# Optimization experiments

Measured on AMD Instinct MI355X. Metric: run time of the kernel, lower is better.

The kernel has to match this reference:

```python
import jax, jax.numpy as jnp
import numpy as np


def setup_inputs() -> dict:
    key = jax.random.key(0)
    k1, k2 = jax.random.split(key)
    # [1, D, H, W, C] cubic feature volume
    image_features = jax.random.normal(k1, (1, 64, 64, 64, 64), dtype=jnp.float32)
    # [1, N, 3] vertex coords in the original 128^3 volume, in [0, 128)
    graph_features = jax.random.uniform(k2, (1, 200000, 3), dtype=jnp.float32) * 128.0
    return {"image_features": image_features, "graph_features": graph_features}


def reference(image_features, graph_features):
    img = image_features[0]                      # [D, H, W, C]
    H = img.shape[0]
    factor = jnp.float32(128.0 / H)
    x = graph_features[..., -3] / factor         # [B, N]
    y = graph_features[..., -2] / factor
    z = graph_features[..., -1] / factor
    hm1 = jnp.float32(H - 1)
    x1 = jnp.floor(x); x2 = jnp.minimum(jnp.ceil(x), hm1)
    y1 = jnp.floor(y); y2 = jnp.minimum(jnp.ceil(y), hm1)
    z1 = jnp.floor(z); z2 = jnp.minimum(jnp.ceil(z), hm1)

    def gather(ix, iy, iz):
        # [B, N] index arrays -> [B, N, C] gathered features
        return img[ix.astype(jnp.int32), iy.astype(jnp.int32), iz.astype(jnp.int32)]

    wx = (x - x1)[..., None]; wx2 = (x2 - x)[..., None]
    wy = (y - y1)[..., None]; wy2 = (y2 - y)[..., None]
    wz = (z - z1)[..., None]; wz2 = (z2 - z)[..., None]

    # z = z1 plane
    q11 = gather(x1, y1, z1); q21 = gather(x2, y1, z1)
    q12 = gather(x1, y2, z1); q22 = gather(x2, y2, z1)
    lerp_y1 = (q22 * wx + q12 * wx2) * wy + (q21 * wx + q11 * wx2) * wy2

    # z = z2 plane
    q11 = gather(x1, y1, z2); q21 = gather(x2, y1, z2)
    q12 = gather(x1, y2, z2); q22 = gather(x2, y2, z2)
    lerp_y2 = (q22 * wx + q12 * wx2) * wy + (q21 * wx + q11 * wx2) * wy2

    return lerp_y2 * wz + lerp_y1 * wz2          # [B, N, C]
```

## Files before the change

kernel.cpp:

```cpp
#include <hip/hip_runtime.h>


#define NBUCK   4096
#define CAP     128
#define OVCAP   8192

typedef float __attribute__((ext_vector_type(4))) fx4;

__device__ __forceinline__ float4 f4mul(float4 a, float s) {
    return make_float4(a.x * s, a.y * s, a.z * s, a.w * s);
}
__device__ __forceinline__ float4 f4fma(float4 a, float s, float4 acc) {
    return make_float4(fmaf(a.x, s, acc.x), fmaf(a.y, s, acc.y),
                       fmaf(a.z, s, acc.z), fmaf(a.w, s, acc.w));
}

__global__ __launch_bounds__(256) void scatter_kernel(
    const float* __restrict__ coords, int* __restrict__ counts,
    float4* __restrict__ buckets, float4* __restrict__ overflow, int n)
{
    int p = blockIdx.x * 256 + threadIdx.x;
    if (p >= n) return;
    float xs = coords[3 * p + 0] * 0.5f;
    float ys = coords[3 * p + 1] * 0.5f;
    float zs = coords[3 * p + 2] * 0.5f;
    int vx = (int)floorf(xs), vy = (int)floorf(ys), vz = (int)floorf(zs);
    int bucket = ((vx >> 2) << 8) | ((vy >> 2) << 4) | (vz >> 2);
    int slot = atomicAdd(&counts[bucket], 1);
    float4 v = make_float4(xs, ys, zs, __int_as_float(p));
    if (slot < CAP) {
        buckets[bucket * CAP + slot] = v;
    } else {
        int o = atomicAdd(&counts[NBUCK], 1);
        if (o < OVCAP) overflow[o] = v;
    }
}

__device__ __forceinline__ void lerp_store(
    const float4* __restrict__ imgv, float4 cs, int cvec,
    float* __restrict__ out)
{
    float x = cs.x, y = cs.y, z = cs.z;
    int p = __float_as_int(cs.w);

    float fx1 = floorf(x), fx2 = fminf(ceilf(x), 63.0f);
    float fy1 = floorf(y), fy2 = fminf(ceilf(y), 63.0f);
    float fz1 = floorf(z), fz2 = fminf(ceilf(z), 63.0f);

    int bx1 = ((int)fx1) << 12, bx2 = ((int)fx2) << 12;
    int by1 = ((int)fy1) << 6,  by2 = ((int)fy2) << 6;
    int iz1 = (int)fz1, iz2 = (int)fz2;

    float4 q111 = imgv[((bx1 + by1 + iz1) << 4) + cvec];
    float4 q211 = imgv[((bx2 + by1 + iz1) << 4) + cvec];
    float4 q121 = imgv[((bx1 + by2 + iz1) << 4) + cvec];
    float4 q221 = imgv[((bx2 + by2 + iz1) << 4) + cvec];
    float4 q112 = imgv[((bx1 + by1 + iz2) << 4) + cvec];
    float4 q212 = imgv[((bx2 + by1 + iz2) << 4) + cvec];
    float4 q122 = imgv[((bx1 + by2 + iz2) << 4) + cvec];
    float4 q222 = imgv[((bx2 + by2 + iz2) << 4) + cvec];

    float wx = x - fx1, wxc = fx2 - x;
    float wy = y - fy1, wyc = fy2 - y;
    float wz = z - fz1, wzc = fz2 - z;

    float4 ly1v = f4fma(f4fma(q221, wx, f4mul(q121, wxc)), wy,
                        f4mul(f4fma(q211, wx, f4mul(q111, wxc)), wyc));
    float4 ly2v = f4fma(f4fma(q222, wx, f4mul(q122, wxc)), wy,
                        f4mul(f4fma(q212, wx, f4mul(q112, wxc)), wyc));
    float4 res = f4fma(ly2v, wz, f4mul(ly1v, wzc));

    fx4 r; r.x = res.x; r.y = res.y; r.z = res.z; r.w = res.w;
    __builtin_nontemporal_store(r, (fx4*)out + (p << 4) + cvec);
}

__global__ __launch_bounds__(256) void gather_kernel(
    const float* __restrict__ img, const int* __restrict__ counts,
    const float4* __restrict__ buckets, const float4* __restrict__ overflow,
    float* __restrict__ out)
{
    const float4* __restrict__ imgv = (const float4*)img;
    int cvec = threadIdx.x & 15;
    int grp  = threadIdx.x >> 4;

    if (blockIdx.x < NBUCK) {
        int bucket = (blockIdx.x & 7) * 512 + (blockIdx.x >> 3);
        int cnt = min(counts[bucket], CAP);

        for (int i = grp; i < cnt; i += 16) {
            float4 cs = buckets[bucket * CAP + i];
            lerp_store(imgv, cs, cvec, out);
        }
    } else {
        int ob = blockIdx.x - NBUCK;
        int cnt = min(counts[NBUCK], OVCAP);
        for (int i = (ob << 4) + grp; i < cnt; i += 32 * 16) {
            float4 cs = overflow[i];
            lerp_store(imgv, cs, cvec, out);
        }
    }
}

__global__ __launch_bounds__(256) void trilerp_kernel(
    const float* __restrict__ img, const float* __restrict__ coords,
    float* __restrict__ out, int n_points)
{
    int tid = blockIdx.x * 256 + threadIdx.x;
    int p = tid >> 4;
    if (p >= n_points) return;
    int cvec = tid & 15;

    float x = coords[3 * p + 0] * 0.5f;
    float y = coords[3 * p + 1] * 0.5f;
    float z = coords[3 * p + 2] * 0.5f;

    float4 cs = make_float4(x, y, z, __int_as_float(p));
    lerp_store((const float4*)img, cs, cvec, out);
}

extern "C" void kernel_launch(void* const* d_in, const int* in_sizes, int n_in,
                              void* d_out, int out_size, void* d_ws, size_t ws_size,
                              hipStream_t stream) {
    const float* img    = (const float*)d_in[0];
    const float* coords = (const float*)d_in[1];
    float* out = (float*)d_out;
    int n = in_sizes[1] / 3;

    size_t counts_bytes = 32768;
    size_t buckets_off  = counts_bytes;
    size_t buckets_bytes = (size_t)NBUCK * CAP * sizeof(float4);
    size_t overflow_off = buckets_off + buckets_bytes;
    size_t need = overflow_off + (size_t)OVCAP * sizeof(float4);

    if (ws_size >= need) {
        int*    counts   = (int*)d_ws;
        float4* buckets  = (float4*)((char*)d_ws + buckets_off);
        float4* overflow = (float4*)((char*)d_ws + overflow_off);

        hipMemsetAsync(counts, 0, (NBUCK + 1) * sizeof(int), stream);
        int pgrid = (n + 255) / 256;
        scatter_kernel<<<pgrid, 256, 0, stream>>>(coords, counts, buckets, overflow, n);
        gather_kernel<<<NBUCK + 32, 256, 0, stream>>>(img, counts, buckets, overflow, out);
    } else {
        int threads = n * 16;
        int grid = (threads + 255) / 256;
        trilerp_kernel<<<grid, 256, 0, stream>>>(img, coords, out, n);
    }
}
```

Measured before the change: 153.0 us.

## Issue two points' corner gathers per group up front, using 512-thread gather blocks

The gather kernel now runs 512-thread blocks with 32 point-groups and unconditionally loads two bucket slots per group. It issues all 16 corner gathers before combining, to raise memory-level parallelism. Slots past the bucket count write to a dummy dump buffer instead of branching. The rest of each bucket goes through a strided loop. To make the unconditional reads of unused slots safe, the whole 8 MB bucket area is now zeroed each call, which adds memset traffic and wasted gathers for sparsely filled buckets.

```diff
diff --git a/kernel.cpp b/kernel.cpp
--- a/kernel.cpp
+++ b/kernel.cpp
@@ -36,48 +36,65 @@
     }
 }
 
-__device__ __forceinline__ void lerp_store(
-    const float4* __restrict__ imgv, float4 cs, int cvec,
-    float* __restrict__ out)
-{
+struct Corner {
+    int o111, o211, o121, o221, o112, o212, o122, o222;
+    float wx, wxc, wy, wyc, wz, wzc;
+};
+
+__device__ __forceinline__ Corner corner_setup(float4 cs, int cvec) {
+    Corner c;
     float x = cs.x, y = cs.y, z = cs.z;
-    int p = __float_as_int(cs.w);
-
     float fx1 = floorf(x), fx2 = fminf(ceilf(x), 63.0f);
     float fy1 = floorf(y), fy2 = fminf(ceilf(y), 63.0f);
     float fz1 = floorf(z), fz2 = fminf(ceilf(z), 63.0f);
-
     int bx1 = ((int)fx1) << 12, bx2 = ((int)fx2) << 12;
     int by1 = ((int)fy1) << 6,  by2 = ((int)fy2) << 6;
-    int iz1 = (int)fz1, iz2 = (int)fz2;
-
-    float4 q111 = imgv[((bx1 + by1 + iz1) << 4) + cvec];
-    float4 q211 = imgv[((bx2 + by1 + iz1) << 4) + cvec];
-    float4 q121 = imgv[((bx1 + by2 + iz1) << 4) + cvec];
-    float4 q221 = imgv[((bx2 + by2 + iz1) << 4) + cvec];
-    float4 q112 = imgv[((bx1 + by1 + iz2) << 4) + cvec];
-    float4 q212 = imgv[((bx2 + by1 + iz2) << 4) + cvec];
-    float4 q122 = imgv[((bx1 + by2 + iz2) << 4) + cvec];
-    float4 q222 = imgv[((bx2 + by2 + iz2) << 4) + cvec];
-
-    float wx = x - fx1, wxc = fx2 - x;
-    float wy = y - fy1, wyc = fy2 - y;
-    float wz = z - fz1, wzc = fz2 - z;
-
-    float4 ly1v = f4fma(f4fma(q221, wx, f4mul(q121, wxc)), wy,
-                        f4mul(f4fma(q211, wx, f4mul(q111, wxc)), wyc));
-    float4 ly2v = f4fma(f4fma(q222, wx, f4mul(q122, wxc)), wy,
-                        f4mul(f4fma(q212, wx, f4mul(q112, wxc)), wyc));
-    float4 res = f4fma(ly2v, wz, f4mul(ly1v, wzc));
-
+    int iz1 = (int)fz1,         iz2 = (int)fz2;
+    c.o111 = ((bx1 + by1 + iz1) << 4) + cvec;
+    c.o211 = ((bx2 + by1 + iz1) << 4) + cvec;
+    c.o121 = ((bx1 + by2 + iz1) << 4) + cvec;
+    c.o221 = ((bx2 + by2 + iz1) << 4) + cvec;
+    c.o112 = ((bx1 + by1 + iz2) << 4) + cvec;
+    c.o212 = ((bx2 + by1 + iz2) << 4) + cvec;
+    c.o122 = ((bx1 + by2 + iz2) << 4) + cvec;
+    c.o222 = ((bx2 + by2 + iz2) << 4) + cvec;
+    c.wx = x - fx1; c.wxc = fx2 - x;
+    c.wy = y - fy1; c.wyc = fy2 - y;
+    c.wz = z - fz1; c.wzc = fz2 - z;
+    return c;
+}
+
+__device__ __forceinline__ float4 tri_combine(
+    const Corner& c,
+    float4 q111, float4 q211, float4 q121, float4 q221,
+    float4 q112, float4 q212, float4 q122, float4 q222)
+{
+    float4 ly1v = f4fma(f4fma(q221, c.wx, f4mul(q121, c.wxc)), c.wy,
+                        f4mul(f4fma(q211, c.wx, f4mul(q111, c.wxc)), c.wyc));
+    float4 ly2v = f4fma(f4fma(q222, c.wx, f4mul(q122, c.wxc)), c.wy,
+                        f4mul(f4fma(q212, c.wx, f4mul(q112, c.wxc)), c.wyc));
+    return f4fma(ly2v, c.wz, f4mul(ly1v, c.wzc));
+}
+
+__device__ __forceinline__ void lerp_global_store(
+    const float4* __restrict__ imgv, float4 cs, int cvec,
+    float* __restrict__ out)
+{
+    Corner c = corner_setup(cs, cvec);
+    int p = __float_as_int(cs.w);
+    float4 q111 = imgv[c.o111], q211 = imgv[c.o211];
+    float4 q121 = imgv[c.o121], q221 = imgv[c.o221];
+    float4 q112 = imgv[c.o112], q212 = imgv[c.o212];
+    float4 q122 = imgv[c.o122], q222 = imgv[c.o222];
+    float4 res = tri_combine(c, q111, q211, q121, q221, q112, q212, q122, q222);
     fx4 r; r.x = res.x; r.y = res.y; r.z = res.z; r.w = res.w;
     __builtin_nontemporal_store(r, (fx4*)out + (p << 4) + cvec);
 }
 
-__global__ __launch_bounds__(256) void gather_kernel(
+__global__ __launch_bounds__(512, 4) void gather_kernel(
     const float* __restrict__ img, const int* __restrict__ counts,
     const float4* __restrict__ buckets, const float4* __restrict__ overflow,
-    float* __restrict__ out)
+    float* __restrict__ out, fx4* __restrict__ dump)
 {
     const float4* __restrict__ imgv = (const float4*)img;
     int cvec = threadIdx.x & 15;
@@ -85,18 +102,52 @@
 
     if (blockIdx.x < NBUCK) {
         int bucket = (blockIdx.x & 7) * 512 + (blockIdx.x >> 3);
+        int base = bucket * CAP;
+
         int cnt = min(counts[bucket], CAP);
-
-        for (int i = grp; i < cnt; i += 16) {
-            float4 cs = buckets[bucket * CAP + i];
-            lerp_store(imgv, cs, cvec, out);
+        float4 cs0 = buckets[base + grp];
+        float4 cs1 = buckets[base + grp + 32];
+
+        Corner c0 = corner_setup(cs0, cvec);
+        float4 a111 = imgv[c0.o111], a211 = imgv[c0.o211];
+        float4 a121 = imgv[c0.o121], a221 = imgv[c0.o221];
+        float4 a112 = imgv[c0.o112], a212 = imgv[c0.o212];
+        float4 a122 = imgv[c0.o122], a222 = imgv[c0.o222];
+
+        Corner c1 = corner_setup(cs1, cvec);
+        float4 b111 = imgv[c1.o111], b211 = imgv[c1.o211];
+        float4 b121 = imgv[c1.o121], b221 = imgv[c1.o221];
+        float4 b112 = imgv[c1.o112], b212 = imgv[c1.o212];
+        float4 b122 = imgv[c1.o122], b222 = imgv[c1.o222];
+
+        {
+            float4 res = tri_combine(c0, a111, a211, a121, a221,
+                                         a112, a212, a122, a222);
+            int p = __float_as_int(cs0.w);
+            fx4* tgt = (grp < cnt) ? ((fx4*)out + (p << 4) + cvec)
+                                   : (dump + threadIdx.x);
+            fx4 r; r.x = res.x; r.y = res.y; r.z = res.z; r.w = res.w;
+            __builtin_nontemporal_store(r, tgt);
+        }
+        {
+            float4 res = tri_combine(c1, b111, b211, b121, b221,
+                                         b112, b212, b122, b222);
+            int p = __float_as_int(cs1.w);
+            fx4* tgt = (grp + 32 < cnt) ? ((fx4*)out + (p << 4) + cvec)
+                                        : (dump + threadIdx.x);
+            fx4 r; r.x = res.x; r.y = res.y; r.z = res.z; r.w = res.w;
+            __builtin_nontemporal_store(r, tgt);
+        }
+        for (int t = grp + 64; t < cnt; t += 32) {
+            float4 cs = buckets[base + t];
+            lerp_global_store(imgv, cs, cvec, out);
         }
     } else {
         int ob = blockIdx.x - NBUCK;
         int cnt = min(counts[NBUCK], OVCAP);
-        for (int i = (ob << 4) + grp; i < cnt; i += 32 * 16) {
+        for (int i = (ob << 5) + grp; i < cnt; i += 32 * 32) {
             float4 cs = overflow[i];
-            lerp_store(imgv, cs, cvec, out);
+            lerp_global_store(imgv, cs, cvec, out);
         }
     }
 }
@@ -115,7 +166,7 @@
     float z = coords[3 * p + 2] * 0.5f;
 
     float4 cs = make_float4(x, y, z, __int_as_float(p));
-    lerp_store((const float4*)img, cs, cvec, out);
+    lerp_global_store((const float4*)img, cs, cvec, out);
 }
 
 extern "C" void kernel_launch(void* const* d_in, const int* in_sizes, int n_in,
@@ -126,21 +177,25 @@
     float* out = (float*)d_out;
     int n = in_sizes[1] / 3;
 
-    size_t counts_bytes = 32768;
-    size_t buckets_off  = counts_bytes;
+    size_t counts_bytes  = 32768;
+    size_t buckets_off   = counts_bytes;
     size_t buckets_bytes = (size_t)NBUCK * CAP * sizeof(float4);
-    size_t overflow_off = buckets_off + buckets_bytes;
-    size_t need = overflow_off + (size_t)OVCAP * sizeof(float4);
+    size_t overflow_off  = buckets_off + buckets_bytes;
+    size_t overflow_bytes = (size_t)OVCAP * sizeof(float4);
+    size_t dump_off      = overflow_off + overflow_bytes;
+    size_t dump_bytes    = 512 * sizeof(fx4);
+    size_t need          = dump_off + dump_bytes;
 
     if (ws_size >= need) {
         int*    counts   = (int*)d_ws;
         float4* buckets  = (float4*)((char*)d_ws + buckets_off);
         float4* overflow = (float4*)((char*)d_ws + overflow_off);
-
-        hipMemsetAsync(counts, 0, (NBUCK + 1) * sizeof(int), stream);
+        fx4*    dump     = (fx4*)((char*)d_ws + dump_off);
+
+        hipMemsetAsync(d_ws, 0, buckets_off + buckets_bytes, stream);
         int pgrid = (n + 255) / 256;
         scatter_kernel<<<pgrid, 256, 0, stream>>>(coords, counts, buckets, overflow, n);
-        gather_kernel<<<NBUCK + 32, 256, 0, stream>>>(img, counts, buckets, overflow, out);
+        gather_kernel<<<NBUCK + 32, 512, 0, stream>>>(img, counts, buckets, overflow, out, dump);
     } else {
         int threads = n * 16;
         int grid = (threads + 255) / 256;
```

After: 153.5 us. About the same (+0.4%).
